# Kernel optimization log

Measured on AMD Instinct MI355X. Metric: run time of the kernel, lower is better.

The kernel has to match this reference:

```python
import jax, jax.numpy as jnp
import numpy as np

HIDDEN = 1024
HEADS = 16
HEAD_DIM = HIDDEN // HEADS
BATCH = 2
SEQ = 2048


def setup_inputs() -> dict:
    key = jax.random.key(0)
    k1, k2, k3 = jax.random.split(key, 3)
    hidden_states = jax.random.normal(k1, (BATCH, SEQ, HIDDEN), dtype=jnp.float32)
    # torch Linear(hidden, 3*hidden) applies x @ W.T; we store the transposed
    # weight directly so the math is x @ W_qkv. Scale ~ fan_in init.
    W_qkv = jax.random.normal(k2, (HIDDEN, 3 * HIDDEN), dtype=jnp.float32) / np.sqrt(HIDDEN)
    W_o = jax.random.normal(k3, (HIDDEN, HIDDEN), dtype=jnp.float32) / np.sqrt(HIDDEN)
    return {"hidden_states": hidden_states, "W_qkv": W_qkv, "W_o": W_o}


def reference(hidden_states, W_qkv, W_o):
    B, S, _ = hidden_states.shape
    scale = 1.0 / np.sqrt(HEAD_DIM)
    qkv = hidden_states @ W_qkv                       # [B, S, 3*H*D]
    qkv = qkv.reshape(B, S, 3, HEADS, HEAD_DIM)
    qkv = jnp.transpose(qkv, (2, 0, 3, 1, 4))         # [3, B, H, S, D]
    q, k, v = qkv[0], qkv[1], qkv[2]
    # The chunked online-softmax path computes exactly softmax(qk^T*scale)v.
    scores = jnp.einsum("bhsd,bhtd->bhst", q, k) * scale  # [B, H, S, S]
    probs = jax.nn.softmax(scores, axis=-1)
    out = jnp.einsum("bhst,bhtd->bhsd", probs, v)     # [B, H, S, D]
    out = jnp.transpose(out, (0, 2, 1, 3)).reshape(B, S, HIDDEN)
    return out @ W_o
```

## Files before the change

### kernel.cpp

```cpp
#include <hip/hip_runtime.h>
#include <hip/hip_bf16.h>
#include <cstdint>

typedef __bf16 bf16_t;
typedef __bf16 bf16x8 __attribute__((ext_vector_type(8)));
typedef __bf16 bf16x4 __attribute__((ext_vector_type(4)));
typedef __bf16 bf16x2 __attribute__((ext_vector_type(2)));
typedef float  f32x4  __attribute__((ext_vector_type(4)));
typedef float  f32x16 __attribute__((ext_vector_type(16)));
typedef unsigned uint4v __attribute__((ext_vector_type(4)));

#define AS1 __attribute__((address_space(1)))
#define AS3 __attribute__((address_space(3)))

static __device__ __forceinline__ void gld_lds16(const void* g, void* l) {
  __builtin_amdgcn_global_load_lds((AS1 void*)g, (AS3 void*)l, 16, 0, 0);
}

static __device__ __forceinline__ unsigned pk2(float a, float b) {
  bf16x2 v; v[0] = (bf16_t)a; v[1] = (bf16_t)b;
  return __builtin_bit_cast(unsigned, v);
}

static __device__ __forceinline__ bf16x8 cat44(bf16x4 a, bf16x4 b) {
  bf16x8 r;
  r[0] = a[0]; r[1] = a[1]; r[2] = a[2]; r[3] = a[3];
  r[4] = b[0]; r[5] = b[1]; r[6] = b[2]; r[7] = b[3];
  return r;
}


__global__ __launch_bounds__(256) void convert_f32_bf16(const float* __restrict__ in,
                                                        bf16_t* __restrict__ out, int n4) {
  int i = blockIdx.x * 256 + threadIdx.x;
  if (i < n4) {
    float4 v = ((const float4*)in)[i];
    bf16x4 o;
    o[0] = (bf16_t)v.x; o[1] = (bf16_t)v.y; o[2] = (bf16_t)v.z; o[3] = (bf16_t)v.w;
    *(bf16x4*)(out + (size_t)i * 4) = o;
  }
}

__global__ __launch_bounds__(256) void transpose_w(const float* __restrict__ in,
                                                   bf16_t* __restrict__ out, int K, int N) {
  __shared__ float tile[32][33];
  const int t = threadIdx.x, c = t & 31, r0 = t >> 5;
  const int bx = blockIdx.x, by = blockIdx.y;
#pragma unroll
  for (int i = 0; i < 4; ++i) {
    int r = r0 + i * 8;
    tile[r][c] = in[(size_t)(by * 32 + r) * N + bx * 32 + c];
  }
  __syncthreads();
#pragma unroll
  for (int i = 0; i < 4; ++i) {
    int r = r0 + i * 8;
    out[(size_t)(bx * 32 + r) * K + by * 32 + c] = (bf16_t)tile[c][r];
  }
}

template <int KDIM>
static __device__ __forceinline__ void gemm128_compute(const bf16_t* __restrict__ A,
                                                       const bf16_t* __restrict__ Bt,
                                                       bf16_t* lA, bf16_t* lB,
                                                       f32x4 acc[4][4],
                                                       int bm, int bn) {
  const int t = threadIdx.x;
  const int lr = t & 15, g = (t >> 4) & 3;
  const int w = t >> 6, wr = w >> 1, wc = w & 1;

  for (int kt = 0; kt < KDIM; kt += 32) {
    __syncthreads();
#pragma unroll
    for (int c2 = 0; c2 < 2; ++c2) {
      const int idx = c2 * 256 + t;
      const int row = idx >> 2, cb = idx & 3;
      const int ldsoff = ((t & 192) + c2 * 256) * 8;
      gld_lds16(A  + (size_t)(bm * 128 + row) * KDIM + kt + cb * 8, lA + ldsoff);
      gld_lds16(Bt + (size_t)(bn * 128 + row) * KDIM + kt + cb * 8, lB + ldsoff);
    }
    __syncthreads();
    bf16x8 af[4], bv[4];
#pragma unroll
    for (int mi = 0; mi < 4; ++mi)
      af[mi] = *(const bf16x8*)(lA + (wr * 64 + mi * 16 + lr) * 32 + g * 8);
#pragma unroll
    for (int ni = 0; ni < 4; ++ni)
      bv[ni] = *(const bf16x8*)(lB + (wc * 64 + ni * 16 + lr) * 32 + g * 8);
#pragma unroll
    for (int mi = 0; mi < 4; ++mi)
#pragma unroll
      for (int ni = 0; ni < 4; ++ni)
        acc[mi][ni] = __builtin_amdgcn_mfma_f32_16x16x32_bf16(af[mi], bv[ni], acc[mi][ni], 0, 0, 0);
  }
}

__global__ __launch_bounds__(256) void gemm_qkv_k(const bf16_t* __restrict__ xb,
                                                  const bf16_t* __restrict__ wt,
                                                  bf16_t* __restrict__ Qo,
                                                  bf16_t* __restrict__ Ko,
                                                  bf16_t* __restrict__ Vto) {
  __shared__ bf16_t lA[128 * 32], lB[128 * 32];
  const int bm = blockIdx.x, bn = blockIdx.y;
  f32x4 acc[4][4] = {};
  gemm128_compute<1024>(xb, wt, lA, lB, acc, bm, bn);
  const float cs = 0.18033688011112042f;
  const int t = threadIdx.x, lr = t & 15, g = (t >> 4) & 3, w = t >> 6, wr = w >> 1, wc = w & 1;
  const int row0 = bm * 128 + wr * 64, col0 = bn * 128 + wc * 64;
#pragma unroll
  for (int mi = 0; mi < 4; ++mi) {
    const int row = row0 + mi * 16 + g * 4;
    const int b = row >> 11, s = row & 2047;
#pragma unroll
    for (int ni = 0; ni < 4; ++ni) {
      const int col = col0 + ni * 16 + lr;
      const int t3 = col >> 10, rem = col & 1023, h = rem >> 6, d = rem & 63;
      const int bh = b * 16 + h;
#pragma unroll
      for (int r = 0; r < 4; ++r) {
        const float av = acc[mi][ni][r];
        if (t3 == 0)      Qo[((size_t)bh * 2048 + s + r) * 64 + d] = (bf16_t)(av * cs);
        else if (t3 == 1) Ko[((size_t)bh * 2048 + s + r) * 64 + d] = (bf16_t)av;
        else              Vto[((size_t)bh * 64 + d) * 2048 + s + r] = (bf16_t)av;
      }
    }
  }
}

__global__ __launch_bounds__(256) void gemm_o_k(const bf16_t* __restrict__ attn,
                                                const bf16_t* __restrict__ wot,
                                                float* __restrict__ out) {
  __shared__ bf16_t lA[128 * 32], lB[128 * 32];
  const int bm = blockIdx.x, bn = blockIdx.y;
  f32x4 acc[4][4] = {};
  gemm128_compute<1024>(attn, wot, lA, lB, acc, bm, bn);
  const int t = threadIdx.x, lr = t & 15, g = (t >> 4) & 3, w = t >> 6, wr = w >> 1, wc = w & 1;
  const int row0 = bm * 128 + wr * 64, col0 = bn * 128 + wc * 64;
#pragma unroll
  for (int mi = 0; mi < 4; ++mi) {
    const int row = row0 + mi * 16 + g * 4;
#pragma unroll
    for (int ni = 0; ni < 4; ++ni) {
      const int col = col0 + ni * 16 + lr;
#pragma unroll
      for (int r = 0; r < 4; ++r)
        out[(size_t)(row + r) * 1024 + col] = acc[mi][ni][r];
    }
  }
}

__global__ __launch_bounds__(256, 2) void attn_k(const bf16_t* __restrict__ Q,
                                                 const bf16_t* __restrict__ K,
                                                 const bf16_t* __restrict__ Vt,
                                                 bf16_t* __restrict__ Ao) {
  __shared__ __align__(16) char smem[32768];
  const int t = threadIdx.x, w = t >> 6, l = t & 63;
  const int ql = l & 31, hi = l >> 5;
  const int orig = blockIdx.y * 16 + blockIdx.x;
  const int swz = (orig & 7) * 64 + (orig >> 3);
  const int qblk = swz & 15, bh = swz >> 4;
  const int b = bh >> 4, h = bh & 15;
  const bf16_t* Qb = Q  + (size_t)bh * 2048 * 64;
  const bf16_t* Kb = K  + (size_t)bh * 2048 * 64;
  const bf16_t* Vb = Vt + (size_t)bh * 64 * 2048;
  const int q0 = qblk * 128 + w * 32;

  const bf16_t* ksrc = Kb + (size_t)l * 64 + w * 8;
  const bf16_t* vsrc = Vb + (size_t)l * 2048 + w * 8;

  const bf16_t* qp = Qb + (size_t)(q0 + ql) * 64 + hi * 8;
  const bf16x8 qf0 = *(const bf16x8*)(qp);
  const bf16x8 qf1 = *(const bf16x8*)(qp + 16);
  const bf16x8 qf2 = *(const bf16x8*)(qp + 32);
  const bf16x8 qf3 = *(const bf16x8*)(qp + 48);

  bf16x8 ones;
#pragma unroll
  for (int i = 0; i < 8; ++i) ones[i] = (bf16_t)1.0f;

  f32x16 ot0 = {}, ot1 = {}, otls = {};

  {
    char* kd = smem;
    gld_lds16(ksrc,      kd + w * 1024);
    gld_lds16(ksrc + 32, kd + (4 + w) * 1024);
    gld_lds16(vsrc,      kd + 8192 + w * 1024);
    gld_lds16(vsrc + 32, kd + 8192 + (4 + w) * 1024);
  }
  __syncthreads();

  for (int jt = 0; jt < 32; ++jt) {
    const int nb = jt & 1;
    const char* kbuf = smem + nb * 16384;
    const char* vbuf = kbuf + 8192;
    if (jt < 31) {
      char* kd = smem + (nb ^ 1) * 16384;
      const bf16_t* ks = ksrc + (size_t)(jt + 1) * 4096;
      const bf16_t* vs = vsrc + (size_t)(jt + 1) * 64;
      gld_lds16(ks,      kd + w * 1024);
      gld_lds16(ks + 32, kd + (4 + w) * 1024);
      gld_lds16(vs,      kd + 8192 + w * 1024);
      gld_lds16(vs + 32, kd + 8192 + (4 + w) * 1024);
    }

    f32x16 s0 = {};
    {
      const bf16x8 ka0 = *(const bf16x8*)(kbuf + (0 + hi) * 1024 + ql * 16);
      const bf16x8 ka1 = *(const bf16x8*)(kbuf + (2 + hi) * 1024 + ql * 16);
      const bf16x8 ka2 = *(const bf16x8*)(kbuf + (4 + hi) * 1024 + ql * 16);
      const bf16x8 ka3 = *(const bf16x8*)(kbuf + (6 + hi) * 1024 + ql * 16);
      s0 = __builtin_amdgcn_mfma_f32_32x32x16_bf16(ka0, qf0, s0, 0, 0, 0);
      s0 = __builtin_amdgcn_mfma_f32_32x32x16_bf16(ka1, qf1, s0, 0, 0, 0);
      s0 = __builtin_amdgcn_mfma_f32_32x32x16_bf16(ka2, qf2, s0, 0, 0, 0);
      s0 = __builtin_amdgcn_mfma_f32_32x32x16_bf16(ka3, qf3, s0, 0, 0, 0);
    }
    f32x16 s1 = {};
    {
      const bf16x8 kb0 = *(const bf16x8*)(kbuf + (0 + hi) * 1024 + 512 + ql * 16);
      const bf16x8 kb1 = *(const bf16x8*)(kbuf + (2 + hi) * 1024 + 512 + ql * 16);
      const bf16x8 kb2 = *(const bf16x8*)(kbuf + (4 + hi) * 1024 + 512 + ql * 16);
      const bf16x8 kb3 = *(const bf16x8*)(kbuf + (6 + hi) * 1024 + 512 + ql * 16);
      s1 = __builtin_amdgcn_mfma_f32_32x32x16_bf16(kb0, qf0, s1, 0, 0, 0);
      s1 = __builtin_amdgcn_mfma_f32_32x32x16_bf16(kb1, qf1, s1, 0, 0, 0);
      s1 = __builtin_amdgcn_mfma_f32_32x32x16_bf16(kb2, qf2, s1, 0, 0, 0);
      s1 = __builtin_amdgcn_mfma_f32_32x32x16_bf16(kb3, qf3, s1, 0, 0, 0);
    }

    bf16x4 va[4], vc[4], vb2[4], vd[4];
#pragma unroll
    for (int i = 0; i < 4; ++i) {
      va[i]  = *(const bf16x4*)(vbuf + i * 1024 + ql * 16 + hi * 8);
      vb2[i] = *(const bf16x4*)(vbuf + i * 1024 + 512 + ql * 16 + hi * 8);
      vc[i]  = *(const bf16x4*)(vbuf + (4 + i) * 1024 + ql * 16 + hi * 8);
      vd[i]  = *(const bf16x4*)(vbuf + (4 + i) * 1024 + 512 + ql * 16 + hi * 8);
    }

    float p0[16], p1[16];
#pragma unroll
    for (int r = 0; r < 16; ++r) p0[r] = exp2f(s0[r]);
#pragma unroll
    for (int r = 0; r < 16; ++r) p1[r] = exp2f(s1[r]);

    uint4v u0 = {pk2(p0[0], p0[1]),  pk2(p0[2], p0[3]),   pk2(p0[4], p0[5]),   pk2(p0[6], p0[7])};
    uint4v u1 = {pk2(p0[8], p0[9]),  pk2(p0[10], p0[11]), pk2(p0[12], p0[13]), pk2(p0[14], p0[15])};
    uint4v u2 = {pk2(p1[0], p1[1]),  pk2(p1[2], p1[3]),   pk2(p1[4], p1[5]),   pk2(p1[6], p1[7])};
    uint4v u3 = {pk2(p1[8], p1[9]),  pk2(p1[10], p1[11]), pk2(p1[12], p1[13]), pk2(p1[14], p1[15])};
    bf16x8 pf0 = __builtin_bit_cast(bf16x8, u0);
    bf16x8 pf1 = __builtin_bit_cast(bf16x8, u1);
    bf16x8 pf2 = __builtin_bit_cast(bf16x8, u2);
    bf16x8 pf3 = __builtin_bit_cast(bf16x8, u3);

    ot0  = __builtin_amdgcn_mfma_f32_32x32x16_bf16(cat44(va[0], va[1]),   pf0, ot0, 0, 0, 0);
    ot1  = __builtin_amdgcn_mfma_f32_32x32x16_bf16(cat44(vb2[0], vb2[1]), pf0, ot1, 0, 0, 0);
    otls = __builtin_amdgcn_mfma_f32_32x32x16_bf16(ones,                  pf0, otls, 0, 0, 0);
    ot0  = __builtin_amdgcn_mfma_f32_32x32x16_bf16(cat44(va[2], va[3]),   pf1, ot0, 0, 0, 0);
    ot1  = __builtin_amdgcn_mfma_f32_32x32x16_bf16(cat44(vb2[2], vb2[3]), pf1, ot1, 0, 0, 0);
    otls = __builtin_amdgcn_mfma_f32_32x32x16_bf16(ones,                  pf1, otls, 0, 0, 0);
    ot0  = __builtin_amdgcn_mfma_f32_32x32x16_bf16(cat44(vc[0], vc[1]),   pf2, ot0, 0, 0, 0);
    ot1  = __builtin_amdgcn_mfma_f32_32x32x16_bf16(cat44(vd[0], vd[1]),   pf2, ot1, 0, 0, 0);
    otls = __builtin_amdgcn_mfma_f32_32x32x16_bf16(ones,                  pf2, otls, 0, 0, 0);
    ot0  = __builtin_amdgcn_mfma_f32_32x32x16_bf16(cat44(vc[2], vc[3]),   pf3, ot0, 0, 0, 0);
    ot1  = __builtin_amdgcn_mfma_f32_32x32x16_bf16(cat44(vd[2], vd[3]),   pf3, ot1, 0, 0, 0);
    otls = __builtin_amdgcn_mfma_f32_32x32x16_bf16(ones,                  pf3, otls, 0, 0, 0);

    __syncthreads();
  }

  const float inv = 1.0f / otls[0];
  bf16_t* ob = (bf16_t*)(smem + w * 4096);
#pragma unroll
  for (int rg = 0; rg < 4; ++rg) {
    const int d0 = rg * 8 + hi * 4;
    bf16x4 v0, v1;
#pragma unroll
    for (int j = 0; j < 4; ++j) {
      v0[j] = (bf16_t)(ot0[4 * rg + j] * inv);
      v1[j] = (bf16_t)(ot1[4 * rg + j] * inv);
    }
    *(bf16x4*)((char*)ob + ql * 128 + (((d0)      * 2) ^ ((ql & 7) << 4))) = v0;
    *(bf16x4*)((char*)ob + ql * 128 + (((d0 + 32) * 2) ^ ((ql & 7) << 4))) = v1;
  }
  __syncthreads();
#pragma unroll
  for (int i = 0; i < 4; ++i) {
    const int c = i * 64 + l;
    const int qq = c >> 3, ch = c & 7;
    bf16x8 vv = *(const bf16x8*)((char*)ob + qq * 128 + ((ch * 16) ^ ((qq & 7) << 4)));
    *(bf16x8*)(Ao + (size_t)(b * 2048 + q0 + qq) * 1024 + h * 64 + ch * 8) = vv;
  }
}


extern "C" void kernel_launch(void* const* d_in, const int* in_sizes, int n_in,
                              void* d_out, int out_size, void* d_ws, size_t ws_size,
                              hipStream_t stream) {
  const float* x    = (const float*)d_in[0];
  const float* wqkv = (const float*)d_in[1];
  const float* wo   = (const float*)d_in[2];
  float* out = (float*)d_out;

  char* ws = (char*)d_ws;
  bf16_t* xb    = (bf16_t*)(ws);
  bf16_t* wqkvT = (bf16_t*)(ws + (size_t)(8u  << 20));
  bf16_t* woT   = (bf16_t*)(ws + (size_t)(14u << 20));
  bf16_t* Qb    = (bf16_t*)(ws + (size_t)(16u << 20));
  bf16_t* Kb    = (bf16_t*)(ws + (size_t)(24u << 20));
  bf16_t* Vtb   = (bf16_t*)(ws + (size_t)(32u << 20));
  bf16_t* attn  = (bf16_t*)(ws + (size_t)(40u << 20));

  convert_f32_bf16<<<4096, 256, 0, stream>>>(x, xb, 4096 * 1024 / 4);
  transpose_w<<<dim3(96, 32), 256, 0, stream>>>(wqkv, wqkvT, 1024, 3072);
  transpose_w<<<dim3(32, 32), 256, 0, stream>>>(wo, woT, 1024, 1024);
  gemm_qkv_k<<<dim3(32, 24), 256, 0, stream>>>(xb, wqkvT, Qb, Kb, Vtb);
  attn_k<<<dim3(16, 32), 256, 0, stream>>>(Qb, Kb, Vtb, attn);
  gemm_o_k<<<dim3(32, 8), 256, 0, stream>>>(attn, woT, out);
}
```

Baseline: 133.7 us.

## Split attention KV range in two with fp32 partials and a combine kernel

Attention is split over the key/value sequence into two halves. This doubles the grid from 512 to 1024 workgroups, and launch bounds are raised to allow 4 waves-groups per SIMD to improve CU occupancy on the large GPU. Each half writes unnormalized fp32 partial outputs and row sums to workspace, and a new combine kernel sums and normalizes them into bf16. No max-subtraction is used, so the partials add directly. This costs an extra launch and about 33 MB of fp32 partial traffic, and it only takes this path if the workspace is large enough.

```diff
diff --git a/kernel.cpp b/kernel.cpp
--- a/kernel.cpp
+++ b/kernel.cpp
@@ -149,20 +149,32 @@
   }
 }
 
-__global__ __launch_bounds__(256, 2) void attn_k(const bf16_t* __restrict__ Q,
-                                                 const bf16_t* __restrict__ K,
-                                                 const bf16_t* __restrict__ Vt,
-                                                 bf16_t* __restrict__ Ao) {
+template <bool PART>
+__global__ __launch_bounds__(256, 4) void attn_k2(const bf16_t* __restrict__ Q,
+                                                  const bf16_t* __restrict__ K,
+                                                  const bf16_t* __restrict__ Vt,
+                                                  float* __restrict__ Opart,
+                                                  float* __restrict__ lpart,
+                                                  bf16_t* __restrict__ Ao) {
   __shared__ __align__(16) char smem[32768];
   const int t = threadIdx.x, w = t >> 6, l = t & 63;
   const int ql = l & 31, hi = l >> 5;
-  const int orig = blockIdx.y * 16 + blockIdx.x;
-  const int swz = (orig & 7) * 64 + (orig >> 3);
-  const int qblk = swz & 15, bh = swz >> 4;
+  int qblk, bh, sp;
+  if constexpr (PART) {
+    const int orig = blockIdx.z * 512 + blockIdx.y * 16 + blockIdx.x;
+    const int swz = (orig & 7) * 128 + (orig >> 3);
+    qblk = swz & 15; bh = (swz >> 4) & 31; sp = swz >> 9;
+  } else {
+    const int orig = blockIdx.y * 16 + blockIdx.x;
+    const int swz = (orig & 7) * 64 + (orig >> 3);
+    qblk = swz & 15; bh = swz >> 4; sp = 0;
+  }
   const int b = bh >> 4, h = bh & 15;
+  const int kvbase = sp * 1024;
+  const int NT = PART ? 16 : 32;
   const bf16_t* Qb = Q  + (size_t)bh * 2048 * 64;
-  const bf16_t* Kb = K  + (size_t)bh * 2048 * 64;
-  const bf16_t* Vb = Vt + (size_t)bh * 64 * 2048;
+  const bf16_t* Kb = K  + (size_t)bh * 2048 * 64 + (size_t)kvbase * 64;
+  const bf16_t* Vb = Vt + (size_t)bh * 64 * 2048 + kvbase;
   const int q0 = qblk * 128 + w * 32;
 
   const bf16_t* ksrc = Kb + (size_t)l * 64 + w * 8;
@@ -189,11 +201,11 @@
   }
   __syncthreads();
 
-  for (int jt = 0; jt < 32; ++jt) {
+  for (int jt = 0; jt < NT; ++jt) {
     const int nb = jt & 1;
     const char* kbuf = smem + nb * 16384;
     const char* vbuf = kbuf + 8192;
-    if (jt < 31) {
+    if (jt < NT - 1) {
       char* kd = smem + (nb ^ 1) * 16384;
       const bf16_t* ks = ksrc + (size_t)(jt + 1) * 4096;
       const bf16_t* vs = vsrc + (size_t)(jt + 1) * 64;
@@ -266,28 +278,64 @@
     __syncthreads();
   }
 
-  const float inv = 1.0f / otls[0];
-  bf16_t* ob = (bf16_t*)(smem + w * 4096);
-#pragma unroll
-  for (int rg = 0; rg < 4; ++rg) {
-    const int d0 = rg * 8 + hi * 4;
-    bf16x4 v0, v1;
-#pragma unroll
-    for (int j = 0; j < 4; ++j) {
-      v0[j] = (bf16_t)(ot0[4 * rg + j] * inv);
-      v1[j] = (bf16_t)(ot1[4 * rg + j] * inv);
-    }
-    *(bf16x4*)((char*)ob + ql * 128 + (((d0)      * 2) ^ ((ql & 7) << 4))) = v0;
-    *(bf16x4*)((char*)ob + ql * 128 + (((d0 + 32) * 2) ^ ((ql & 7) << 4))) = v1;
-  }
-  __syncthreads();
-#pragma unroll
-  for (int i = 0; i < 4; ++i) {
-    const int c = i * 64 + l;
-    const int qq = c >> 3, ch = c & 7;
-    bf16x8 vv = *(const bf16x8*)((char*)ob + qq * 128 + ((ch * 16) ^ ((qq & 7) << 4)));
-    *(bf16x8*)(Ao + (size_t)(b * 2048 + q0 + qq) * 1024 + h * 64 + ch * 8) = vv;
-  }
+  if constexpr (PART) {
+    float* ob = (float*)(smem + w * 8192);
+#pragma unroll
+    for (int rg = 0; rg < 4; ++rg) {
+      const int d0 = rg * 8 + hi * 4;
+      f32x4 v0 = {ot0[4 * rg + 0], ot0[4 * rg + 1], ot0[4 * rg + 2], ot0[4 * rg + 3]};
+      f32x4 v1 = {ot1[4 * rg + 0], ot1[4 * rg + 1], ot1[4 * rg + 2], ot1[4 * rg + 3]};
+      *(f32x4*)((char*)ob + ql * 256 + (((d0)      * 4) ^ ((ql & 15) << 4))) = v0;
+      *(f32x4*)((char*)ob + ql * 256 + (((d0 + 32) * 4) ^ ((ql & 15) << 4))) = v1;
+    }
+    __syncthreads();
+    const size_t rowbase = (size_t)(sp * 32 + bh) * 2048 + q0;
+#pragma unroll
+    for (int i = 0; i < 8; ++i) {
+      const int c = i * 64 + l;
+      const int qq = c >> 4, ch = c & 15;
+      f32x4 vv = *(const f32x4*)((char*)ob + qq * 256 + ((ch * 16) ^ ((qq & 15) << 4)));
+      *(f32x4*)(Opart + (rowbase + qq) * 64 + ch * 4) = vv;
+    }
+    if (hi == 0) lpart[rowbase + ql] = otls[0];
+  } else {
+    const float inv = 1.0f / otls[0];
+    bf16_t* ob = (bf16_t*)(smem + w * 4096);
+#pragma unroll
+    for (int rg = 0; rg < 4; ++rg) {
+      const int d0 = rg * 8 + hi * 4;
+      bf16x4 v0, v1;
+#pragma unroll
+      for (int j = 0; j < 4; ++j) {
+        v0[j] = (bf16_t)(ot0[4 * rg + j] * inv);
+        v1[j] = (bf16_t)(ot1[4 * rg + j] * inv);
+      }
+      *(bf16x4*)((char*)ob + ql * 128 + (((d0)      * 2) ^ ((ql & 7) << 4))) = v0;
+      *(bf16x4*)((char*)ob + ql * 128 + (((d0 + 32) * 2) ^ ((ql & 7) << 4))) = v1;
+    }
+    __syncthreads();
+#pragma unroll
+    for (int i = 0; i < 4; ++i) {
+      const int c = i * 64 + l;
+      const int qq = c >> 3, ch = c & 7;
+      bf16x8 vv = *(const bf16x8*)((char*)ob + qq * 128 + ((ch * 16) ^ ((qq & 7) << 4)));
+      *(bf16x8*)(Ao + (size_t)(b * 2048 + q0 + qq) * 1024 + h * 64 + ch * 8) = vv;
+    }
+  }
+}
+
+__global__ __launch_bounds__(256) void attn_combine(const float* __restrict__ Opart,
+                                                    const float* __restrict__ lpart,
+                                                    bf16_t* __restrict__ Ao) {
+  const int R = blockIdx.x * 4 + (threadIdx.x >> 6);
+  const int d = threadIdx.x & 63;
+  const int bh = R >> 11, q = R & 2047, b = bh >> 4, h = bh & 15;
+  const size_t NPo = (size_t)32 * 2048 * 64;
+  const size_t NPl = (size_t)32 * 2048;
+  const float inv = 1.0f / (lpart[R] + lpart[NPl + R]);
+  const float o0 = Opart[(size_t)R * 64 + d];
+  const float o1 = Opart[NPo + (size_t)R * 64 + d];
+  Ao[((size_t)b * 2048 + q) * 1024 + h * 64 + d] = (bf16_t)((o0 + o1) * inv);
 }
 
 
@@ -307,11 +355,20 @@
   bf16_t* Kb    = (bf16_t*)(ws + (size_t)(24u << 20));
   bf16_t* Vtb   = (bf16_t*)(ws + (size_t)(32u << 20));
   bf16_t* attn  = (bf16_t*)(ws + (size_t)(40u << 20));
+  float*  Opart = (float*)(ws + (size_t)(48u << 20));
+  float*  lpart = (float*)(ws + (size_t)(80u << 20));
 
   convert_f32_bf16<<<4096, 256, 0, stream>>>(x, xb, 4096 * 1024 / 4);
   transpose_w<<<dim3(96, 32), 256, 0, stream>>>(wqkv, wqkvT, 1024, 3072);
   transpose_w<<<dim3(32, 32), 256, 0, stream>>>(wo, woT, 1024, 1024);
   gemm_qkv_k<<<dim3(32, 24), 256, 0, stream>>>(xb, wqkvT, Qb, Kb, Vtb);
-  attn_k<<<dim3(16, 32), 256, 0, stream>>>(Qb, Kb, Vtb, attn);
+
+  if (ws_size >= ((size_t)81u << 20)) {
+    attn_k2<true><<<dim3(16, 32, 2), 256, 0, stream>>>(Qb, Kb, Vtb, Opart, lpart, nullptr);
+    attn_combine<<<16384, 256, 0, stream>>>(Opart, lpart, attn);
+  } else {
+    attn_k2<false><<<dim3(16, 32), 256, 0, stream>>>(Qb, Kb, Vtb, nullptr, nullptr, attn);
+  }
+
   gemm_o_k<<<dim3(32, 8), 256, 0, stream>>>(attn, woT, out);
 }
```

Result: slower. 144.7 us (+8.2%).

## Software-pipeline QK of next tile with softmax-PV, permute V layout, truncating pack

Applied to the files above, without the earlier changes.

Restructures the attention loop so that the QK^T MFMAs for tile j+1 are issued alongside the exp/PV work for tile j. K is staged two tiles ahead and V one tile ahead, in separate K and V double buffers. The V-transpose store in the QKV GEMM now permutes key positions so PV operands load as single 16-byte LDS reads instead of concatenating four-element halves. The fp32-to-bf16 pack becomes a single byte-permute that truncates rather than rounds, which slightly changes numerics. The cost is more live registers for the in-flight score accumulators, which may reduce occupancy.

```diff
diff --git a/kernel.cpp b/kernel.cpp
--- a/kernel.cpp
+++ b/kernel.cpp
@@ -17,16 +17,9 @@
   __builtin_amdgcn_global_load_lds((AS1 void*)g, (AS3 void*)l, 16, 0, 0);
 }
 
-static __device__ __forceinline__ unsigned pk2(float a, float b) {
-  bf16x2 v; v[0] = (bf16_t)a; v[1] = (bf16_t)b;
-  return __builtin_bit_cast(unsigned, v);
-}
-
-static __device__ __forceinline__ bf16x8 cat44(bf16x4 a, bf16x4 b) {
-  bf16x8 r;
-  r[0] = a[0]; r[1] = a[1]; r[2] = a[2]; r[3] = a[3];
-  r[4] = b[0]; r[5] = b[1]; r[6] = b[2]; r[7] = b[3];
-  return r;
+static __device__ __forceinline__ unsigned pk2t(float a, float b) {
+  return __builtin_amdgcn_perm(__builtin_bit_cast(unsigned, a),
+                               __builtin_bit_cast(unsigned, b), 0x03020706u);
 }
 
 
@@ -121,7 +114,13 @@
         const float av = acc[mi][ni][r];
         if (t3 == 0)      Qo[((size_t)bh * 2048 + s + r) * 64 + d] = (bf16_t)(av * cs);
         else if (t3 == 1) Ko[((size_t)bh * 2048 + s + r) * 64 + d] = (bf16_t)av;
-        else              Vto[((size_t)bh * 64 + d) * 2048 + s + r] = (bf16_t)av;
+        else {
+          const int kv = s + r;
+          const int q3 = (kv >> 2) & 7;
+          const int dq = (q3 & 4) | ((q3 & 1) << 1) | ((q3 >> 1) & 1);
+          const int kvp = (kv & ~31) | (dq << 2) | (kv & 3);
+          Vto[((size_t)bh * 64 + d) * 2048 + kvp] = (bf16_t)av;
+        }
       }
     }
   }
@@ -168,6 +167,11 @@
   const bf16_t* ksrc = Kb + (size_t)l * 64 + w * 8;
   const bf16_t* vsrc = Vb + (size_t)l * 2048 + w * 8;
 
+  char* const kb0 = smem;
+  char* const kb1 = smem + 8192;
+  char* const vb0 = smem + 16384;
+  char* const vb1 = smem + 24576;
+
   const bf16_t* qp = Qb + (size_t)(q0 + ql) * 64 + hi * 8;
   const bf16x8 qf0 = *(const bf16x8*)(qp);
   const bf16x8 qf1 = *(const bf16x8*)(qp + 16);
@@ -180,90 +184,91 @@
 
   f32x16 ot0 = {}, ot1 = {}, otls = {};
 
-  {
-    char* kd = smem;
-    gld_lds16(ksrc,      kd + w * 1024);
-    gld_lds16(ksrc + 32, kd + (4 + w) * 1024);
-    gld_lds16(vsrc,      kd + 8192 + w * 1024);
-    gld_lds16(vsrc + 32, kd + 8192 + (4 + w) * 1024);
-  }
+  auto stageK = [&](int tile, char* dst) {
+    const bf16_t* ks = ksrc + (size_t)tile * 4096;
+    gld_lds16(ks,      dst + w * 1024);
+    gld_lds16(ks + 32, dst + (4 + w) * 1024);
+  };
+  auto stageV = [&](int tile, char* dst) {
+    const bf16_t* vs = vsrc + (size_t)tile * 64;
+    gld_lds16(vs,      dst + w * 1024);
+    gld_lds16(vs + 32, dst + (4 + w) * 1024);
+  };
+  auto qk = [&](const char* kbuf, f32x16& sa, f32x16& sb) {
+    const bf16x8 ka0 = *(const bf16x8*)(kbuf + (0 + hi) * 1024 + ql * 16);
+    const bf16x8 ka1 = *(const bf16x8*)(kbuf + (2 + hi) * 1024 + ql * 16);
+    const bf16x8 ka2 = *(const bf16x8*)(kbuf + (4 + hi) * 1024 + ql * 16);
+    const bf16x8 ka3 = *(const bf16x8*)(kbuf + (6 + hi) * 1024 + ql * 16);
+    sa = __builtin_amdgcn_mfma_f32_32x32x16_bf16(ka0, qf0, sa, 0, 0, 0);
+    sa = __builtin_amdgcn_mfma_f32_32x32x16_bf16(ka1, qf1, sa, 0, 0, 0);
+    sa = __builtin_amdgcn_mfma_f32_32x32x16_bf16(ka2, qf2, sa, 0, 0, 0);
+    sa = __builtin_amdgcn_mfma_f32_32x32x16_bf16(ka3, qf3, sa, 0, 0, 0);
+    const bf16x8 kb0f = *(const bf16x8*)(kbuf + (0 + hi) * 1024 + 512 + ql * 16);
+    const bf16x8 kb1f = *(const bf16x8*)(kbuf + (2 + hi) * 1024 + 512 + ql * 16);
+    const bf16x8 kb2f = *(const bf16x8*)(kbuf + (4 + hi) * 1024 + 512 + ql * 16);
+    const bf16x8 kb3f = *(const bf16x8*)(kbuf + (6 + hi) * 1024 + 512 + ql * 16);
+    sb = __builtin_amdgcn_mfma_f32_32x32x16_bf16(kb0f, qf0, sb, 0, 0, 0);
+    sb = __builtin_amdgcn_mfma_f32_32x32x16_bf16(kb1f, qf1, sb, 0, 0, 0);
+    sb = __builtin_amdgcn_mfma_f32_32x32x16_bf16(kb2f, qf2, sb, 0, 0, 0);
+    sb = __builtin_amdgcn_mfma_f32_32x32x16_bf16(kb3f, qf3, sb, 0, 0, 0);
+  };
+  auto sm_pv = [&](const f32x16& sa, const f32x16& sb, const char* vread) {
+    uint4v u0 = {pk2t(exp2f(sa[0]),  exp2f(sa[1])),  pk2t(exp2f(sa[2]),  exp2f(sa[3])),
+                 pk2t(exp2f(sa[4]),  exp2f(sa[5])),  pk2t(exp2f(sa[6]),  exp2f(sa[7]))};
+    uint4v u1 = {pk2t(exp2f(sa[8]),  exp2f(sa[9])),  pk2t(exp2f(sa[10]), exp2f(sa[11])),
+                 pk2t(exp2f(sa[12]), exp2f(sa[13])), pk2t(exp2f(sa[14]), exp2f(sa[15]))};
+    uint4v u2 = {pk2t(exp2f(sb[0]),  exp2f(sb[1])),  pk2t(exp2f(sb[2]),  exp2f(sb[3])),
+                 pk2t(exp2f(sb[4]),  exp2f(sb[5])),  pk2t(exp2f(sb[6]),  exp2f(sb[7]))};
+    uint4v u3 = {pk2t(exp2f(sb[8]),  exp2f(sb[9])),  pk2t(exp2f(sb[10]), exp2f(sb[11])),
+                 pk2t(exp2f(sb[12]), exp2f(sb[13])), pk2t(exp2f(sb[14]), exp2f(sb[15]))};
+    const bf16x8 pf0 = __builtin_bit_cast(bf16x8, u0);
+    const bf16x8 pf1 = __builtin_bit_cast(bf16x8, u1);
+    const bf16x8 pf2 = __builtin_bit_cast(bf16x8, u2);
+    const bf16x8 pf3 = __builtin_bit_cast(bf16x8, u3);
+    const bf16x8 v00 = *(const bf16x8*)(vread + (0 + hi) * 1024 + ql * 16);
+    const bf16x8 v01 = *(const bf16x8*)(vread + (2 + hi) * 1024 + ql * 16);
+    const bf16x8 v02 = *(const bf16x8*)(vread + (4 + hi) * 1024 + ql * 16);
+    const bf16x8 v03 = *(const bf16x8*)(vread + (6 + hi) * 1024 + ql * 16);
+    const bf16x8 v10 = *(const bf16x8*)(vread + (0 + hi) * 1024 + 512 + ql * 16);
+    const bf16x8 v11 = *(const bf16x8*)(vread + (2 + hi) * 1024 + 512 + ql * 16);
+    const bf16x8 v12 = *(const bf16x8*)(vread + (4 + hi) * 1024 + 512 + ql * 16);
+    const bf16x8 v13 = *(const bf16x8*)(vread + (6 + hi) * 1024 + 512 + ql * 16);
+    ot0  = __builtin_amdgcn_mfma_f32_32x32x16_bf16(v00,  pf0, ot0, 0, 0, 0);
+    ot1  = __builtin_amdgcn_mfma_f32_32x32x16_bf16(v10,  pf0, ot1, 0, 0, 0);
+    otls = __builtin_amdgcn_mfma_f32_32x32x16_bf16(ones, pf0, otls, 0, 0, 0);
+    ot0  = __builtin_amdgcn_mfma_f32_32x32x16_bf16(v01,  pf1, ot0, 0, 0, 0);
+    ot1  = __builtin_amdgcn_mfma_f32_32x32x16_bf16(v11,  pf1, ot1, 0, 0, 0);
+    otls = __builtin_amdgcn_mfma_f32_32x32x16_bf16(ones, pf1, otls, 0, 0, 0);
+    ot0  = __builtin_amdgcn_mfma_f32_32x32x16_bf16(v02,  pf2, ot0, 0, 0, 0);
+    ot1  = __builtin_amdgcn_mfma_f32_32x32x16_bf16(v12,  pf2, ot1, 0, 0, 0);
+    otls = __builtin_amdgcn_mfma_f32_32x32x16_bf16(ones, pf2, otls, 0, 0, 0);
+    ot0  = __builtin_amdgcn_mfma_f32_32x32x16_bf16(v03,  pf3, ot0, 0, 0, 0);
+    ot1  = __builtin_amdgcn_mfma_f32_32x32x16_bf16(v13,  pf3, ot1, 0, 0, 0);
+    otls = __builtin_amdgcn_mfma_f32_32x32x16_bf16(ones, pf3, otls, 0, 0, 0);
+  };
+
+  stageK(0, kb0);
+  stageV(0, vb0);
+  stageK(1, kb1);
   __syncthreads();
-
-  for (int jt = 0; jt < 32; ++jt) {
-    const int nb = jt & 1;
-    const char* kbuf = smem + nb * 16384;
-    const char* vbuf = kbuf + 8192;
-    if (jt < 31) {
-      char* kd = smem + (nb ^ 1) * 16384;
-      const bf16_t* ks = ksrc + (size_t)(jt + 1) * 4096;
-      const bf16_t* vs = vsrc + (size_t)(jt + 1) * 64;
-      gld_lds16(ks,      kd + w * 1024);
-      gld_lds16(ks + 32, kd + (4 + w) * 1024);
-      gld_lds16(vs,      kd + 8192 + w * 1024);
-      gld_lds16(vs + 32, kd + 8192 + (4 + w) * 1024);
-    }
-
-    f32x16 s0 = {};
-    {
-      const bf16x8 ka0 = *(const bf16x8*)(kbuf + (0 + hi) * 1024 + ql * 16);
-      const bf16x8 ka1 = *(const bf16x8*)(kbuf + (2 + hi) * 1024 + ql * 16);
-      const bf16x8 ka2 = *(const bf16x8*)(kbuf + (4 + hi) * 1024 + ql * 16);
-      const bf16x8 ka3 = *(const bf16x8*)(kbuf + (6 + hi) * 1024 + ql * 16);
-      s0 = __builtin_amdgcn_mfma_f32_32x32x16_bf16(ka0, qf0, s0, 0, 0, 0);
-      s0 = __builtin_amdgcn_mfma_f32_32x32x16_bf16(ka1, qf1, s0, 0, 0, 0);
-      s0 = __builtin_amdgcn_mfma_f32_32x32x16_bf16(ka2, qf2, s0, 0, 0, 0);
-      s0 = __builtin_amdgcn_mfma_f32_32x32x16_bf16(ka3, qf3, s0, 0, 0, 0);
-    }
-    f32x16 s1 = {};
-    {
-      const bf16x8 kb0 = *(const bf16x8*)(kbuf + (0 + hi) * 1024 + 512 + ql * 16);
-      const bf16x8 kb1 = *(const bf16x8*)(kbuf + (2 + hi) * 1024 + 512 + ql * 16);
-      const bf16x8 kb2 = *(const bf16x8*)(kbuf + (4 + hi) * 1024 + 512 + ql * 16);
-      const bf16x8 kb3 = *(const bf16x8*)(kbuf + (6 + hi) * 1024 + 512 + ql * 16);
-      s1 = __builtin_amdgcn_mfma_f32_32x32x16_bf16(kb0, qf0, s1, 0, 0, 0);
-      s1 = __builtin_amdgcn_mfma_f32_32x32x16_bf16(kb1, qf1, s1, 0, 0, 0);
-      s1 = __builtin_amdgcn_mfma_f32_32x32x16_bf16(kb2, qf2, s1, 0, 0, 0);
-      s1 = __builtin_amdgcn_mfma_f32_32x32x16_bf16(kb3, qf3, s1, 0, 0, 0);
-    }
-
-    bf16x4 va[4], vc[4], vb2[4], vd[4];
-#pragma unroll
-    for (int i = 0; i < 4; ++i) {
-      va[i]  = *(const bf16x4*)(vbuf + i * 1024 + ql * 16 + hi * 8);
-      vb2[i] = *(const bf16x4*)(vbuf + i * 1024 + 512 + ql * 16 + hi * 8);
-      vc[i]  = *(const bf16x4*)(vbuf + (4 + i) * 1024 + ql * 16 + hi * 8);
-      vd[i]  = *(const bf16x4*)(vbuf + (4 + i) * 1024 + 512 + ql * 16 + hi * 8);
-    }
-
-    float p0[16], p1[16];
-#pragma unroll
-    for (int r = 0; r < 16; ++r) p0[r] = exp2f(s0[r]);
-#pragma unroll
-    for (int r = 0; r < 16; ++r) p1[r] = exp2f(s1[r]);
-
-    uint4v u0 = {pk2(p0[0], p0[1]),  pk2(p0[2], p0[3]),   pk2(p0[4], p0[5]),   pk2(p0[6], p0[7])};
-    uint4v u1 = {pk2(p0[8], p0[9]),  pk2(p0[10], p0[11]), pk2(p0[12], p0[13]), pk2(p0[14], p0[15])};
-    uint4v u2 = {pk2(p1[0], p1[1]),  pk2(p1[2], p1[3]),   pk2(p1[4], p1[5]),   pk2(p1[6], p1[7])};
-    uint4v u3 = {pk2(p1[8], p1[9]),  pk2(p1[10], p1[11]), pk2(p1[12], p1[13]), pk2(p1[14], p1[15])};
-    bf16x8 pf0 = __builtin_bit_cast(bf16x8, u0);
-    bf16x8 pf1 = __builtin_bit_cast(bf16x8, u1);
-    bf16x8 pf2 = __builtin_bit_cast(bf16x8, u2);
-    bf16x8 pf3 = __builtin_bit_cast(bf16x8, u3);
-
-    ot0  = __builtin_amdgcn_mfma_f32_32x32x16_bf16(cat44(va[0], va[1]),   pf0, ot0, 0, 0, 0);
-    ot1  = __builtin_amdgcn_mfma_f32_32x32x16_bf16(cat44(vb2[0], vb2[1]), pf0, ot1, 0, 0, 0);
-    otls = __builtin_amdgcn_mfma_f32_32x32x16_bf16(ones,                  pf0, otls, 0, 0, 0);
-    ot0  = __builtin_amdgcn_mfma_f32_32x32x16_bf16(cat44(va[2], va[3]),   pf1, ot0, 0, 0, 0);
-    ot1  = __builtin_amdgcn_mfma_f32_32x32x16_bf16(cat44(vb2[2], vb2[3]), pf1, ot1, 0, 0, 0);
-    otls = __builtin_amdgcn_mfma_f32_32x32x16_bf16(ones,                  pf1, otls, 0, 0, 0);
-    ot0  = __builtin_amdgcn_mfma_f32_32x32x16_bf16(cat44(vc[0], vc[1]),   pf2, ot0, 0, 0, 0);
-    ot1  = __builtin_amdgcn_mfma_f32_32x32x16_bf16(cat44(vd[0], vd[1]),   pf2, ot1, 0, 0, 0);
-    otls = __builtin_amdgcn_mfma_f32_32x32x16_bf16(ones,                  pf2, otls, 0, 0, 0);
-    ot0  = __builtin_amdgcn_mfma_f32_32x32x16_bf16(cat44(vc[2], vc[3]),   pf3, ot0, 0, 0, 0);
-    ot1  = __builtin_amdgcn_mfma_f32_32x32x16_bf16(cat44(vd[2], vd[3]),   pf3, ot1, 0, 0, 0);
-    otls = __builtin_amdgcn_mfma_f32_32x32x16_bf16(ones,                  pf3, otls, 0, 0, 0);
-
+  f32x16 sca = {}, scb = {};
+  qk(kb0, sca, scb);
+  __syncthreads();
+
+  auto body = [&](int j, char* kstage, const char* kread, const char* vread, char* vstage) {
+    if (j < 30) stageK(j + 2, kstage);
+    if (j < 31) stageV(j + 1, vstage);
+    f32x16 sna = {}, snb = {};
+    if (j < 31) qk(kread, sna, snb);
+    sm_pv(sca, scb, vread);
     __syncthreads();
+    sca = sna; scb = snb;
+  };
+
+#pragma unroll 2
+  for (int j = 0; j < 32; ++j) {
+    if ((j & 1) == 0) body(j, kb0, kb1, vb0, vb1);
+    else              body(j, kb1, kb0, vb1, vb0);
   }
 
   const float inv = 1.0f / otls[0];
```

Result: no change. 131.7 us (-1.5%).
